# Optimization experiments

Hardware: AMD Instinct MI355X
Metric: run time of the kernel (lower is better)

The kernel has to match this reference:

```python
import jax, jax.numpy as jnp
import numpy as np

B, DIN, DOUT, NW = 32768, 768, 768, 48
NH = NW // 3  # num_haar == num_mexican == num_morlet == 16 for NW=48
OMEGA0 = 5.0
LN_EPS = 1e-5


def setup_inputs() -> dict:
    key = jax.random.key(0)
    ks = jax.random.split(key, 6)
    x = jax.random.normal(ks[0], (B, DIN), dtype=jnp.float32)
    # kaiming-normal-ish fan_in init for linear layers, zero bias
    W = jax.random.normal(ks[1], (DOUT, DIN), dtype=jnp.float32) / np.sqrt(DIN)
    b = jnp.zeros((DOUT,), jnp.float32)
    Wp = jax.random.normal(ks[2], (NW, DIN), dtype=jnp.float32) / np.sqrt(DIN)
    bp = jnp.zeros((NW,), jnp.float32)
    Wc = jax.random.normal(ks[3], (DOUT, NW), dtype=jnp.float32) / np.sqrt(NW)
    bc = jnp.zeros((DOUT,), jnp.float32)
    # mixed-type init: per-family logspace scales / linspace translations
    scales = jnp.asarray(np.concatenate([
        np.logspace(-0.5, 0.5, NH),
        np.logspace(-0.3, 0.7, NH),
        np.logspace(-0.3, 0.7, NW - 2 * NH)]), jnp.float32)
    translations = jnp.asarray(np.concatenate([
        np.linspace(-1.5, 1.5, NH),
        np.linspace(-1.5, 1.5, NH),
        np.linspace(-1.5, 1.5, NW - 2 * NH)]), jnp.float32)
    gamma = jnp.ones((DOUT,), jnp.float32)
    beta = jnp.zeros((DOUT,), jnp.float32)
    return {"x": x, "W": W, "b": b, "Wp": Wp, "bp": bp, "Wc": Wc,
            "bc": bc, "scales": scales, "translations": translations,
            "gamma": gamma, "beta": beta}


def _wavelet_basis(s):
    # s: [B, NW] already scaled/translated; columns split by family
    dt = s.dtype
    sh = s[:, :NH]
    haar = (((sh >= 0) & (sh < 0.5)).astype(dt)
            - ((sh >= 0.5) & (sh < 1.0)).astype(dt))
    sm = s[:, NH:2 * NH]
    mexican = (1.0 - sm * sm) * jnp.exp(-0.5 * sm * sm)
    so = s[:, 2 * NH:]
    morlet = jnp.cos(OMEGA0 * so) * jnp.exp(-0.5 * so * so)
    return jnp.concatenate([haar, mexican, morlet], axis=1)


def reference(x, W, b, Wp, bp, Wc, bc, scales, translations, gamma, beta):
    direct = x @ W.T + b                              # [B, DOUT]
    wi = x @ Wp.T + bp                                # [B, NW]
    s = (wi - translations) / scales                  # [B, NW]
    wav = jax.nn.gelu(_wavelet_basis(s), approximate=False)
    wpath = wav @ Wc.T + bc                           # [B, DOUT]
    h = direct + wpath
    mu = jnp.mean(h, axis=-1, keepdims=True)
    var = jnp.mean((h - mu) ** 2, axis=-1, keepdims=True)
    return (h - mu) * jax.lax.rsqrt(var + LN_EPS) * gamma + beta
```

## Files before the change

kernel.cpp:

```cpp
#include <hip/hip_runtime.h>
#include <math.h>


#define B_SZ  32768
#define DIN   768
#define DOUT  768
#define NWAV  48

#define WF_OFF   0
#define WPH_OFF  589824
#define WPL_OFF  638976
#define WCF_OFF  688128

typedef short bf16x8 __attribute__((ext_vector_type(8)));
typedef float f32x16 __attribute__((ext_vector_type(16)));

__device__ __forceinline__ float bf2f(short u) {
    union { unsigned int i; float f; } v;
    v.i = ((unsigned int)(unsigned short)u) << 16;
    return v.f;
}
__device__ __forceinline__ short f2bf(float f) {
    union { float f; unsigned int i; } v; v.f = f;
    unsigned int r = v.i + 0x7FFFu + ((v.i >> 16) & 1u);
    return (short)(r >> 16);
}

__global__ __launch_bounds__(256) void pack_kernel(
    const float* __restrict__ W, const float* __restrict__ Wp,
    const float* __restrict__ Wc, short* __restrict__ ws)
{
    const int gw = (blockIdx.x * 256 + threadIdx.x) >> 6;
    const int L  = threadIdx.x & 63;
    const int lm = L & 31, half = L >> 5;

    if (gw < 1152) {
        const int cb = gw / 48, kb = gw % 48;
        const int row = cb * 32 + lm;
        const int k = kb * 16 + half * 8;
        bf16x8 o;
#pragma unroll
        for (int j = 0; j < 8; j++) o[j] = f2bf(W[(size_t)row * DIN + k + j]);
        *reinterpret_cast<bf16x8*>(&ws[WF_OFF + (size_t)gw * 512 + L * 8]) = o;
    } else if (gw < 1248) {
        const int t = gw - 1152;
        const int ct = t / 48, kb = t % 48;
        const int j = ct * 32 + lm;
        const int k = kb * 16 + half * 8;
        bf16x8 h, l;
#pragma unroll
        for (int jj = 0; jj < 8; jj++) {
            float v = (j < NWAV) ? Wp[(size_t)j * DIN + k + jj] : 0.f;
            const short hh = f2bf(v);
            h[jj] = hh;
            l[jj] = f2bf(v - bf2f(hh));
        }
        *reinterpret_cast<bf16x8*>(&ws[WPH_OFF + (size_t)t * 512 + L * 8]) = h;
        *reinterpret_cast<bf16x8*>(&ws[WPL_OFF + (size_t)t * 512 + L * 8]) = l;
    } else if (gw < 1320) {
        const int t = gw - 1248;
        const int cb = t / 3, kb = t % 3;
        const int row = cb * 32 + lm;
        const int k = kb * 16 + half * 8;
        bf16x8 o;
#pragma unroll
        for (int jj = 0; jj < 8; jj++) o[jj] = f2bf(Wc[(size_t)row * NWAV + k + jj]);
        *reinterpret_cast<bf16x8*>(&ws[WCF_OFF + (size_t)t * 512 + L * 8]) = o;
    }
}

__global__ __launch_bounds__(512, 2) void fused_kernel(
    const float* __restrict__ x, const short* __restrict__ ws,
    const float* __restrict__ Wp,
    const float* __restrict__ bp, const float* __restrict__ sc,
    const float* __restrict__ tr,
    const float* __restrict__ bb, const float* __restrict__ bc,
    const float* __restrict__ gm, const float* __restrict__ bt,
    float* __restrict__ out)
{
    __shared__ __align__(16) short xh[2][64 * 72];
    __shared__ __align__(16) short xl[2][64 * 72];
    __shared__ float redS[64 * 8], redQ[64 * 8];
    __shared__ float muA[64], rsA[64];
    __shared__ unsigned flags[64];
    __shared__ double dred[8];

    const short* WF  = ws + WF_OFF;
    const short* WPH = ws + WPH_OFF;
    const short* WPL = ws + WPL_OFF;
    const short* WCF = ws + WCF_OFF;

    const int tid = threadIdx.x;
    const int r0  = blockIdx.x * 64;
    const int L   = tid & 63;
    const int wv  = __builtin_amdgcn_readfirstlane(tid >> 6);
    const int lm  = L & 31, half = L >> 5;
    const int L8  = L * 8;
    const bool wi = (wv < 4);
    const int wv3 = wv * 3;
    const int wrt = wv & 1, wct = wv >> 1;
    const int wct48 = wct * 48;

    if (tid < 64) flags[tid] = 0u;

    f32x16 acc[2][3];
#pragma unroll
    for (int rt = 0; rt < 2; rt++)
#pragma unroll
        for (int ct = 0; ct < 3; ct++)
#pragma unroll
            for (int g = 0; g < 16; g++) acc[rt][ct][g] = 0.f;
    f32x16 wacc;
#pragma unroll
    for (int g = 0; g < 16; g++) wacc[g] = 0.f;

    const int srow = tid >> 3;
    const int sk   = (tid & 7) * 8;

    {
        const float4* xp = reinterpret_cast<const float4*>(&x[(size_t)(r0 + srow) * DIN + sk]);
        const float4 v0 = xp[0], v1 = xp[1];
        const float f[8] = {v0.x, v0.y, v0.z, v0.w, v1.x, v1.y, v1.z, v1.w};
        bf16x8 hh, ll;
#pragma unroll
        for (int i = 0; i < 8; i++) {
            const short h = f2bf(f[i]);
            hh[i] = h;
            ll[i] = f2bf(f[i] - bf2f(h));
        }
        *reinterpret_cast<bf16x8*>(&xh[0][srow * 72 + sk]) = hh;
        *reinterpret_cast<bf16x8*>(&xl[0][srow * 72 + sk]) = ll;
    }
    __syncthreads();

    for (int k0i = 0; k0i < 12; ++k0i) {
        const int cur = k0i & 1;
        const int kb0 = k0i * 4;

        float4 v0, v1;
        if (k0i < 11) {
            const float4* xp = reinterpret_cast<const float4*>(
                &x[(size_t)(r0 + srow) * DIN + (k0i + 1) * 64 + sk]);
            v0 = xp[0]; v1 = xp[1];
        }

        bf16x8 bfr[4][3];
#pragma unroll
        for (int ks = 0; ks < 4; ++ks)
#pragma unroll
            for (int ct = 0; ct < 3; ++ct)
                bfr[ks][ct] = *reinterpret_cast<const bf16x8*>(
                    &WF[((size_t)((wv3 + ct) * 48 + kb0 + ks)) * 512 + L8]);
        bf16x8 bwh[4], bwl[4];
        if (wi) {
#pragma unroll
            for (int ks = 0; ks < 4; ++ks) {
                bwh[ks] = *reinterpret_cast<const bf16x8*>(
                    &WPH[((size_t)(wct48 + kb0 + ks)) * 512 + L8]);
                bwl[ks] = *reinterpret_cast<const bf16x8*>(
                    &WPL[((size_t)(wct48 + kb0 + ks)) * 512 + L8]);
            }
        }

#pragma unroll
        for (int ks = 0; ks < 4; ++ks) {
            const bf16x8 a0 = *reinterpret_cast<bf16x8*>(
                &xh[cur][lm * 72 + ks * 16 + half * 8]);
            const bf16x8 a1 = *reinterpret_cast<bf16x8*>(
                &xh[cur][(32 + lm) * 72 + ks * 16 + half * 8]);
#pragma unroll
            for (int ct = 0; ct < 3; ++ct) {
                acc[0][ct] = __builtin_amdgcn_mfma_f32_32x32x16_bf16(a0, bfr[ks][ct], acc[0][ct], 0, 0, 0);
                acc[1][ct] = __builtin_amdgcn_mfma_f32_32x32x16_bf16(a1, bfr[ks][ct], acc[1][ct], 0, 0, 0);
            }
            if (wi) {
                const bf16x8 ah = wrt ? a1 : a0;
                const bf16x8 al = *reinterpret_cast<bf16x8*>(
                    &xl[cur][(wrt * 32 + lm) * 72 + ks * 16 + half * 8]);
                wacc = __builtin_amdgcn_mfma_f32_32x32x16_bf16(ah, bwl[ks], wacc, 0, 0, 0);
                wacc = __builtin_amdgcn_mfma_f32_32x32x16_bf16(al, bwh[ks], wacc, 0, 0, 0);
                wacc = __builtin_amdgcn_mfma_f32_32x32x16_bf16(ah, bwh[ks], wacc, 0, 0, 0);
            }
        }

        if (k0i < 11) {
            const float f[8] = {v0.x, v0.y, v0.z, v0.w, v1.x, v1.y, v1.z, v1.w};
            bf16x8 hh, ll;
#pragma unroll
            for (int i = 0; i < 8; i++) {
                const short h = f2bf(f[i]);
                hh[i] = h;
                ll[i] = f2bf(f[i] - bf2f(h));
            }
            *reinterpret_cast<bf16x8*>(&xh[1 - cur][srow * 72 + sk]) = hh;
            *reinterpret_cast<bf16x8*>(&xl[1 - cur][srow * 72 + sk]) = ll;
        }
        __syncthreads();
    }

    short* wavL = &xh[0][0];
    if (wi) {
        const int j = wct * 32 + lm;
        if (j < NWAV) {
            const float bpv = bp[j], scv = sc[j], trv = tr[j];
#pragma unroll
            for (int g = 0; g < 16; ++g) {
                const int rowl = wrt * 32 + (g & 3) + 8 * (g >> 2) + 4 * half;
                const float wiv = wacc[g] + bpv;
                const float s = (wiv - trv) / scv;
                float w;
                if (j < 16) {
                    const float dmin = fminf(fabsf(s), fminf(fabsf(s - 0.5f), fabsf(s - 1.0f)));
                    if (dmin < 2e-4f) atomicOr(&flags[rowl], 1u << j);
                    w = (s >= 0.f && s < 0.5f) ? 1.f : ((s >= 0.5f && s < 1.f) ? -1.f : 0.f);
                } else if (j < 32) {
                    w = (1.f - s * s) * expf(-0.5f * s * s);
                } else {
                    w = cosf(5.f * s) * expf(-0.5f * s * s);
                }
                const float gel = 0.5f * w * (1.f + erff(w * 0.70710678118654752f));
                wavL[rowl * 72 + j] = f2bf(gel);
            }
        }
    }
    __syncthreads();

#pragma unroll 1
    for (int fr = 0; fr < 64; ++fr) {
        unsigned m = flags[fr];
        while (m) {
            const int j = __ffs(m) - 1;
            m &= m - 1;
            const float* xr = &x[(size_t)(r0 + fr) * DIN];
            const float* wr = &Wp[(size_t)j * DIN];
            double a = (double)xr[tid] * (double)wr[tid];
            if (tid < DIN - 512)
                a += (double)xr[tid + 512] * (double)wr[tid + 512];
            a += __shfl_xor(a, 1);  a += __shfl_xor(a, 2);
            a += __shfl_xor(a, 4);  a += __shfl_xor(a, 8);
            a += __shfl_xor(a, 16); a += __shfl_xor(a, 32);
            if (L == 0) dred[wv] = a;
            __syncthreads();
            if (tid == 0) {
                double wid = (double)bp[j];
#pragma unroll
                for (int i = 0; i < 8; i++) wid += dred[i];
                const double sd = (wid - (double)tr[j]) / (double)sc[j];
                const double w = (sd >= 0.0 && sd < 0.5) ? 1.0
                               : ((sd >= 0.5 && sd < 1.0) ? -1.0 : 0.0);
                const double gel = 0.5 * w * (1.0 + erf(w * 0.70710678118654752));
                wavL[fr * 72 + j] = f2bf((float)gel);
            }
            __syncthreads();
        }
    }

#pragma unroll
    for (int ks = 0; ks < 3; ++ks) {
        const bf16x8 a0 = *reinterpret_cast<bf16x8*>(&wavL[lm * 72 + ks * 16 + half * 8]);
        const bf16x8 a1 = *reinterpret_cast<bf16x8*>(&wavL[(32 + lm) * 72 + ks * 16 + half * 8]);
#pragma unroll
        for (int ct = 0; ct < 3; ++ct) {
            const bf16x8 b = *reinterpret_cast<const bf16x8*>(
                &WCF[((size_t)((wv3 + ct) * 3 + ks)) * 512 + L8]);
            acc[0][ct] = __builtin_amdgcn_mfma_f32_32x32x16_bf16(a0, b, acc[0][ct], 0, 0, 0);
            acc[1][ct] = __builtin_amdgcn_mfma_f32_32x32x16_bf16(a1, b, acc[1][ct], 0, 0, 0);
        }
    }

    float bias[3], gmv[3], btv[3];
#pragma unroll
    for (int ct = 0; ct < 3; ++ct) {
        const int col = wv * 96 + ct * 32 + lm;
        bias[ct] = bb[col] + bc[col];
        gmv[ct] = gm[col];
        btv[ct] = bt[col];
    }
#pragma unroll
    for (int rt = 0; rt < 2; ++rt) {
#pragma unroll
        for (int g = 0; g < 16; ++g) {
            const float v0 = acc[rt][0][g] + bias[0];
            const float v1 = acc[rt][1][g] + bias[1];
            const float v2 = acc[rt][2][g] + bias[2];
            acc[rt][0][g] = v0; acc[rt][1][g] = v1; acc[rt][2][g] = v2;
            float s1 = v0 + v1 + v2;
            float s2 = v0 * v0 + v1 * v1 + v2 * v2;
            s1 += __shfl_xor(s1, 1);  s2 += __shfl_xor(s2, 1);
            s1 += __shfl_xor(s1, 2);  s2 += __shfl_xor(s2, 2);
            s1 += __shfl_xor(s1, 4);  s2 += __shfl_xor(s2, 4);
            s1 += __shfl_xor(s1, 8);  s2 += __shfl_xor(s2, 8);
            s1 += __shfl_xor(s1, 16); s2 += __shfl_xor(s2, 16);
            if (lm == 0) {
                const int rowl = rt * 32 + (g & 3) + 8 * (g >> 2) + 4 * half;
                redS[rowl * 8 + wv] = s1;
                redQ[rowl * 8 + wv] = s2;
            }
        }
    }
    __syncthreads();
    if (tid < 64) {
        float S = 0.f, Q = 0.f;
#pragma unroll
        for (int i = 0; i < 8; i++) { S += redS[tid * 8 + i]; Q += redQ[tid * 8 + i]; }
        const float mu = S * (1.f / 768.f);
        const float var = Q * (1.f / 768.f) - mu * mu;
        muA[tid] = mu;
        rsA[tid] = rsqrtf(var + 1e-5f);
    }
    __syncthreads();

#pragma unroll
    for (int rt = 0; rt < 2; ++rt) {
#pragma unroll
        for (int g = 0; g < 16; ++g) {
            const int rowl = rt * 32 + (g & 3) + 8 * (g >> 2) + 4 * half;
            const float mu = muA[rowl], rs = rsA[rowl];
            float* orow = &out[(size_t)(r0 + rowl) * DOUT + wv * 96 + lm];
#pragma unroll
            for (int ct = 0; ct < 3; ++ct) {
                orow[ct * 32] = (acc[rt][ct][g] - mu) * rs * gmv[ct] + btv[ct];
            }
        }
    }
}

extern "C" void kernel_launch(void* const* d_in, const int* in_sizes, int n_in,
                              void* d_out, int out_size, void* d_ws, size_t ws_size,
                              hipStream_t stream)
{
    const float* x  = (const float*)d_in[0];
    const float* W  = (const float*)d_in[1];
    const float* b  = (const float*)d_in[2];
    const float* Wp = (const float*)d_in[3];
    const float* bp = (const float*)d_in[4];
    const float* Wc = (const float*)d_in[5];
    const float* bc = (const float*)d_in[6];
    const float* sc = (const float*)d_in[7];
    const float* tr = (const float*)d_in[8];
    const float* gm = (const float*)d_in[9];
    const float* bt = (const float*)d_in[10];
    float* out = (float*)d_out;
    short* ws  = (short*)d_ws;

    pack_kernel<<<dim3(330), dim3(256), 0, stream>>>(W, Wp, Wc, ws);
    fused_kernel<<<dim3(B_SZ / 64), dim3(512), 0, stream>>>(
        x, ws, Wp, bp, sc, tr, b, bc, gm, bt, out);
}
```

Before: 267.8 us.

## Process two K-chunks per barrier with four-slot LDS ring buffer

Expands the x staging buffers in LDS from two slots to four and restructures the K loop so each iteration handles two 64-wide K chunks before a single barrier. This halves the number of __syncthreads calls and gives a longer prefetch distance for the x loads. In exchange it doubles LDS use for the staging buffers and raises register pressure from holding two sets of weight fragments and prefetched x values, which may hurt occupancy under launch_bounds(512,2).

```diff
diff --git a/kernel.cpp b/kernel.cpp
--- a/kernel.cpp
+++ b/kernel.cpp
@@ -78,8 +78,8 @@
     const float* __restrict__ gm, const float* __restrict__ bt,
     float* __restrict__ out)
 {
-    __shared__ __align__(16) short xh[2][64 * 72];
-    __shared__ __align__(16) short xl[2][64 * 72];
+    __shared__ __align__(16) short xh[4][64 * 72];
+    __shared__ __align__(16) short xl[4][64 * 72];
     __shared__ float redS[64 * 8], redQ[64 * 8];
     __shared__ float muA[64], rsA[64];
     __shared__ unsigned flags[64];
@@ -117,8 +117,10 @@
     const int srow = tid >> 3;
     const int sk   = (tid & 7) * 8;
 
-    {
-        const float4* xp = reinterpret_cast<const float4*>(&x[(size_t)(r0 + srow) * DIN + sk]);
+#pragma unroll
+    for (int c = 0; c < 2; ++c) {
+        const float4* xp = reinterpret_cast<const float4*>(
+            &x[(size_t)(r0 + srow) * DIN + c * 64 + sk]);
         const float4 v0 = xp[0], v1 = xp[1];
         const float f[8] = {v0.x, v0.y, v0.z, v0.w, v1.x, v1.y, v1.z, v1.w};
         bf16x8 hh, ll;
@@ -128,72 +130,133 @@
             hh[i] = h;
             ll[i] = f2bf(f[i] - bf2f(h));
         }
-        *reinterpret_cast<bf16x8*>(&xh[0][srow * 72 + sk]) = hh;
-        *reinterpret_cast<bf16x8*>(&xl[0][srow * 72 + sk]) = ll;
+        *reinterpret_cast<bf16x8*>(&xh[c][srow * 72 + sk]) = hh;
+        *reinterpret_cast<bf16x8*>(&xl[c][srow * 72 + sk]) = ll;
     }
     __syncthreads();
 
-    for (int k0i = 0; k0i < 12; ++k0i) {
-        const int cur = k0i & 1;
-        const int kb0 = k0i * 4;
-
-        float4 v0, v1;
-        if (k0i < 11) {
+    for (int s = 0; s < 6; ++s) {
+        const int kA = 2 * s, kB = 2 * s + 1;
+        const int bA = kA & 3, bB = kB & 3;
+        const int kbA = kA * 4, kbB = kB * 4;
+
+        bf16x8 bfrA[4][3];
+#pragma unroll
+        for (int ks = 0; ks < 4; ++ks)
+#pragma unroll
+            for (int ct = 0; ct < 3; ++ct)
+                bfrA[ks][ct] = *reinterpret_cast<const bf16x8*>(
+                    &WF[((size_t)((wv3 + ct) * 48 + kbA + ks)) * 512 + L8]);
+        bf16x8 bwhA[4], bwlA[4];
+        if (wi) {
+#pragma unroll
+            for (int ks = 0; ks < 4; ++ks) {
+                bwhA[ks] = *reinterpret_cast<const bf16x8*>(
+                    &WPH[((size_t)(wct48 + kbA + ks)) * 512 + L8]);
+                bwlA[ks] = *reinterpret_cast<const bf16x8*>(
+                    &WPL[((size_t)(wct48 + kbA + ks)) * 512 + L8]);
+            }
+        }
+        float4 vA0, vA1;
+        if (s < 5) {
             const float4* xp = reinterpret_cast<const float4*>(
-                &x[(size_t)(r0 + srow) * DIN + (k0i + 1) * 64 + sk]);
-            v0 = xp[0]; v1 = xp[1];
-        }
-
-        bf16x8 bfr[4][3];
-#pragma unroll
-        for (int ks = 0; ks < 4; ++ks)
-#pragma unroll
-            for (int ct = 0; ct < 3; ++ct)
-                bfr[ks][ct] = *reinterpret_cast<const bf16x8*>(
-                    &WF[((size_t)((wv3 + ct) * 48 + kb0 + ks)) * 512 + L8]);
-        bf16x8 bwh[4], bwl[4];
-        if (wi) {
-#pragma unroll
-            for (int ks = 0; ks < 4; ++ks) {
-                bwh[ks] = *reinterpret_cast<const bf16x8*>(
-                    &WPH[((size_t)(wct48 + kb0 + ks)) * 512 + L8]);
-                bwl[ks] = *reinterpret_cast<const bf16x8*>(
-                    &WPL[((size_t)(wct48 + kb0 + ks)) * 512 + L8]);
-            }
+                &x[(size_t)(r0 + srow) * DIN + (kA + 2) * 64 + sk]);
+            vA0 = xp[0]; vA1 = xp[1];
         }
 
 #pragma unroll
         for (int ks = 0; ks < 4; ++ks) {
             const bf16x8 a0 = *reinterpret_cast<bf16x8*>(
-                &xh[cur][lm * 72 + ks * 16 + half * 8]);
+                &xh[bA][lm * 72 + ks * 16 + half * 8]);
             const bf16x8 a1 = *reinterpret_cast<bf16x8*>(
-                &xh[cur][(32 + lm) * 72 + ks * 16 + half * 8]);
+                &xh[bA][(32 + lm) * 72 + ks * 16 + half * 8]);
 #pragma unroll
             for (int ct = 0; ct < 3; ++ct) {
-                acc[0][ct] = __builtin_amdgcn_mfma_f32_32x32x16_bf16(a0, bfr[ks][ct], acc[0][ct], 0, 0, 0);
-                acc[1][ct] = __builtin_amdgcn_mfma_f32_32x32x16_bf16(a1, bfr[ks][ct], acc[1][ct], 0, 0, 0);
+                acc[0][ct] = __builtin_amdgcn_mfma_f32_32x32x16_bf16(a0, bfrA[ks][ct], acc[0][ct], 0, 0, 0);
+                acc[1][ct] = __builtin_amdgcn_mfma_f32_32x32x16_bf16(a1, bfrA[ks][ct], acc[1][ct], 0, 0, 0);
             }
             if (wi) {
                 const bf16x8 ah = wrt ? a1 : a0;
                 const bf16x8 al = *reinterpret_cast<bf16x8*>(
-                    &xl[cur][(wrt * 32 + lm) * 72 + ks * 16 + half * 8]);
-                wacc = __builtin_amdgcn_mfma_f32_32x32x16_bf16(ah, bwl[ks], wacc, 0, 0, 0);
-                wacc = __builtin_amdgcn_mfma_f32_32x32x16_bf16(al, bwh[ks], wacc, 0, 0, 0);
-                wacc = __builtin_amdgcn_mfma_f32_32x32x16_bf16(ah, bwh[ks], wacc, 0, 0, 0);
-            }
-        }
-
-        if (k0i < 11) {
-            const float f[8] = {v0.x, v0.y, v0.z, v0.w, v1.x, v1.y, v1.z, v1.w};
-            bf16x8 hh, ll;
-#pragma unroll
-            for (int i = 0; i < 8; i++) {
-                const short h = f2bf(f[i]);
-                hh[i] = h;
-                ll[i] = f2bf(f[i] - bf2f(h));
-            }
-            *reinterpret_cast<bf16x8*>(&xh[1 - cur][srow * 72 + sk]) = hh;
-            *reinterpret_cast<bf16x8*>(&xl[1 - cur][srow * 72 + sk]) = ll;
+                    &xl[bA][(wrt * 32 + lm) * 72 + ks * 16 + half * 8]);
+                wacc = __builtin_amdgcn_mfma_f32_32x32x16_bf16(ah, bwlA[ks], wacc, 0, 0, 0);
+                wacc = __builtin_amdgcn_mfma_f32_32x32x16_bf16(al, bwhA[ks], wacc, 0, 0, 0);
+                wacc = __builtin_amdgcn_mfma_f32_32x32x16_bf16(ah, bwhA[ks], wacc, 0, 0, 0);
+            }
+        }
+
+        bf16x8 bfrB[4][3];
+#pragma unroll
+        for (int ks = 0; ks < 4; ++ks)
+#pragma unroll
+            for (int ct = 0; ct < 3; ++ct)
+                bfrB[ks][ct] = *reinterpret_cast<const bf16x8*>(
+                    &WF[((size_t)((wv3 + ct) * 48 + kbB + ks)) * 512 + L8]);
+        bf16x8 bwhB[4], bwlB[4];
+        if (wi) {
+#pragma unroll
+            for (int ks = 0; ks < 4; ++ks) {
+                bwhB[ks] = *reinterpret_cast<const bf16x8*>(
+                    &WPH[((size_t)(wct48 + kbB + ks)) * 512 + L8]);
+                bwlB[ks] = *reinterpret_cast<const bf16x8*>(
+                    &WPL[((size_t)(wct48 + kbB + ks)) * 512 + L8]);
+            }
+        }
+        float4 vB0, vB1;
+        if (s < 5) {
+            const float4* xp = reinterpret_cast<const float4*>(
+                &x[(size_t)(r0 + srow) * DIN + (kB + 2) * 64 + sk]);
+            vB0 = xp[0]; vB1 = xp[1];
+        }
+
+#pragma unroll
+        for (int ks = 0; ks < 4; ++ks) {
+            const bf16x8 a0 = *reinterpret_cast<bf16x8*>(
+                &xh[bB][lm * 72 + ks * 16 + half * 8]);
+            const bf16x8 a1 = *reinterpret_cast<bf16x8*>(
+                &xh[bB][(32 + lm) * 72 + ks * 16 + half * 8]);
+#pragma unroll
+            for (int ct = 0; ct < 3; ++ct) {
+                acc[0][ct] = __builtin_amdgcn_mfma_f32_32x32x16_bf16(a0, bfrB[ks][ct], acc[0][ct], 0, 0, 0);
+                acc[1][ct] = __builtin_amdgcn_mfma_f32_32x32x16_bf16(a1, bfrB[ks][ct], acc[1][ct], 0, 0, 0);
+            }
+            if (wi) {
+                const bf16x8 ah = wrt ? a1 : a0;
+                const bf16x8 al = *reinterpret_cast<bf16x8*>(
+                    &xl[bB][(wrt * 32 + lm) * 72 + ks * 16 + half * 8]);
+                wacc = __builtin_amdgcn_mfma_f32_32x32x16_bf16(ah, bwlB[ks], wacc, 0, 0, 0);
+                wacc = __builtin_amdgcn_mfma_f32_32x32x16_bf16(al, bwhB[ks], wacc, 0, 0, 0);
+                wacc = __builtin_amdgcn_mfma_f32_32x32x16_bf16(ah, bwhB[ks], wacc, 0, 0, 0);
+            }
+        }
+
+        if (s < 5) {
+            {
+                const float f[8] = {vA0.x, vA0.y, vA0.z, vA0.w, vA1.x, vA1.y, vA1.z, vA1.w};
+                bf16x8 hh, ll;
+#pragma unroll
+                for (int i = 0; i < 8; i++) {
+                    const short h = f2bf(f[i]);
+                    hh[i] = h;
+                    ll[i] = f2bf(f[i] - bf2f(h));
+                }
+                const int bn = (kA + 2) & 3;
+                *reinterpret_cast<bf16x8*>(&xh[bn][srow * 72 + sk]) = hh;
+                *reinterpret_cast<bf16x8*>(&xl[bn][srow * 72 + sk]) = ll;
+            }
+            {
+                const float f[8] = {vB0.x, vB0.y, vB0.z, vB0.w, vB1.x, vB1.y, vB1.z, vB1.w};
+                bf16x8 hh, ll;
+#pragma unroll
+                for (int i = 0; i < 8; i++) {
+                    const short h = f2bf(f[i]);
+                    hh[i] = h;
+                    ll[i] = f2bf(f[i] - bf2f(h));
+                }
+                const int bn = (kB + 2) & 3;
+                *reinterpret_cast<bf16x8*>(&xh[bn][srow * 72 + sk]) = hh;
+                *reinterpret_cast<bf16x8*>(&xl[bn][srow * 72 + sk]) = ll;
+            }
         }
         __syncthreads();
     }
```

After: 265.9 us. No clear change (-0.7%).
